# Kernel optimization log

Measured on AMD Instinct MI355X. Metric: run time of the kernel, lower is better.

## Reference

```python
import jax, jax.numpy as jnp
import numpy as np

N_NODES = 100000
N_EDGES = 1600000
DIM_IN, DIM_HID, DIM_OUT = 256, 128, 64


def _gcn_norm(edge_index, num_nodes):
    # PyG gcn_norm with add_self_loops=True, symmetric normalization.
    loop = jnp.arange(num_nodes, dtype=edge_index.dtype)
    row = jnp.concatenate([edge_index[0], loop])  # source
    col = jnp.concatenate([edge_index[1], loop])  # destination
    deg = jax.ops.segment_sum(jnp.ones_like(col, dtype=jnp.float32), col,
                              num_segments=num_nodes)
    dis = jnp.where(deg > 0, jax.lax.rsqrt(deg), 0.0)
    norm = dis[row] * dis[col]  # [E + N]
    return row, col, norm


def _gcn_conv(x, row, col, norm, W, b, num_nodes):
    h = x @ W                      # [N, d_out] linear first (d_out <= d_in typical)
    msg = h[row] * norm[:, None]   # gather + edge scaling, [E+N, d_out]
    out = jax.ops.segment_sum(msg, col, num_segments=num_nodes)  # scatter-add
    return out + b


def setup_inputs() -> dict:
    key = jax.random.key(0)
    k1, k2, k3, k4, k5 = jax.random.split(key, 5)
    x = jax.random.normal(k1, (N_NODES, DIM_IN), dtype=jnp.float32)
    edge_index = jax.random.randint(k2, (2, N_EDGES), 0, N_NODES, dtype=jnp.int32)
    s1 = 1.0 / np.sqrt(DIM_IN)
    s2 = 1.0 / np.sqrt(DIM_HID)
    W1 = jax.random.uniform(k3, (DIM_IN, DIM_HID), jnp.float32, -s1, s1)
    b1 = jnp.zeros((DIM_HID,), jnp.float32)
    W2 = jax.random.uniform(k4, (DIM_HID, DIM_OUT), jnp.float32, -s2, s2)
    b2 = jnp.zeros((DIM_OUT,), jnp.float32)
    return {"x": x, "edge_index": edge_index, "W1": W1, "b1": b1,
            "W2": W2, "b2": b2}


def reference(x, edge_index, W1, b1, W2, b2):
    n = x.shape[0]
    row, col, norm = _gcn_norm(edge_index, n)  # cached=True: shared by both layers
    h = _gcn_conv(x, row, col, norm, W1, b1, n)
    h = jax.nn.relu(h)
    h = _gcn_conv(h, row, col, norm, W2, b2, n)
    return jax.nn.log_softmax(h, axis=-1)
```

## Files before the change

### kernel.cpp

```cpp
#include <hip/hip_runtime.h>

#define N_NODES 100000
#define N_EDGES 1600000
#define DIN 256
#define DHID 128
#define DOUT 64

#define BSHIFT 8
#define NBUCKET ((N_NODES + 255) / 256)
#define CHUNK 4096
#define NCHUNK ((N_EDGES + CHUNK - 1) / CHUNK)

typedef __attribute__((ext_vector_type(8))) short bf16x8;
typedef __attribute__((ext_vector_type(4))) float f32x4;
typedef __attribute__((ext_vector_type(2))) float f32x2;

static __device__ __forceinline__ ushort f2bf(float f) {
  union { float f; uint u; } a; a.f = f;
  uint u = a.u;
  uint r = u + 0x7fffu + ((u >> 16) & 1u);
  return (ushort)(r >> 16);
}


#if __has_builtin(__builtin_amdgcn_cvt_pk_f32_fp8) && __has_builtin(__builtin_amdgcn_cvt_pk_fp8_f32) && __has_builtin(__builtin_amdgcn_cvt_f32_fp8)
#define FP8_HW 1
#else
#define FP8_HW 0
#endif

static __device__ __forceinline__ uint f2fp8(float f) {
#if FP8_HW
  return (uint)(__builtin_amdgcn_cvt_pk_fp8_f32(f, f, 0, false) & 0xFF);
#else
  uint u = __float_as_uint(f);
  uint s = (u >> 24) & 0x80u;
  u &= 0x7FFFFFFFu;
  u += 0x7FFFFu + ((u >> 20) & 1u);
  int e = (int)(u >> 23) - 120;
  uint m = (u >> 20) & 7u;
  uint v = (e <= 0) ? 0u : ((e >= 15) ? 0x7Eu : (((uint)e << 3) | m));
  return s | v;
#endif
}

static __device__ __forceinline__ f32x2 fp8x2f(uint v) {
#if FP8_HW
  return __builtin_amdgcn_cvt_pk_f32_fp8(v, false);
#else
  uint lo = v & 0xFFu, hi = (v >> 8) & 0xFFu;
  uint mlo = lo & 0x7Fu, mhi = hi & 0x7Fu;
  uint blo = (mlo ? ((mlo << 4) + 0x3C00u) : 0u) | ((lo & 0x80u) << 8);
  uint bhi = (mhi ? ((mhi << 4) + 0x3C00u) : 0u) | ((hi & 0x80u) << 8);
  f32x2 r;
  r.x = __uint_as_float(blo << 16);
  r.y = __uint_as_float(bhi << 16);
  return r;
#endif
}


__global__ __launch_bounds__(256) void k_hist(const int* __restrict__ colp,
                                              int* __restrict__ cntmat) {
  __shared__ int h[NBUCKET];
  int c = blockIdx.x;
  for (int i = threadIdx.x; i < NBUCKET; i += 256) h[i] = 0;
  __syncthreads();
  int e0 = c * CHUNK, e1 = min(e0 + CHUNK, N_EDGES);
  for (int e = e0 + threadIdx.x; e < e1; e += 256)
    atomicAdd(&h[colp[e] >> BSHIFT], 1);
  __syncthreads();
  for (int i = threadIdx.x; i < NBUCKET; i += 256)
    cntmat[c * NBUCKET + i] = h[i];
}


__global__ __launch_bounds__(256) void k_buckettot(const int* __restrict__ cntmat,
                                                   int* __restrict__ btot) {
  __shared__ int s[256];
  int b = blockIdx.x, t = threadIdx.x;
  int sum = 0;
  for (int c = t; c < NCHUNK; c += 256) sum += cntmat[c * NBUCKET + b];
  s[t] = sum;
  __syncthreads();
  for (int d = 128; d > 0; d >>= 1) {
    if (t < d) s[t] += s[t + d];
    __syncthreads();
  }
  if (t == 0) btot[b] = s[0];
}


__global__ void k_bucketscan(const int* __restrict__ btot, int* __restrict__ bbase) {
  __shared__ int s[256];
  int t = threadIdx.x;
  int b0 = 2 * t, b1 = 2 * t + 1;
  int v0 = (b0 < NBUCKET) ? btot[b0] : 0;
  int v1 = (b1 < NBUCKET) ? btot[b1] : 0;
  int ps = v0 + v1;
  s[t] = ps;
  __syncthreads();
  for (int d = 1; d < 256; d <<= 1) {
    int y = (t >= d) ? s[t - d] : 0;
    __syncthreads();
    s[t] += y;
    __syncthreads();
  }
  int ex = s[t] - ps;
  if (b0 < NBUCKET) bbase[b0] = ex;
  if (b1 < NBUCKET) bbase[b1] = ex + v0;
  if (t == 0) bbase[NBUCKET] = N_EDGES;
}


__global__ __launch_bounds__(256) void k_chunkpfx(const int* __restrict__ cntmat,
                                                  const int* __restrict__ bbase,
                                                  int* __restrict__ basemat) {
  int wid = blockIdx.x * 4 + (threadIdx.x >> 6);
  int lane = threadIdx.x & 63;
  if (wid >= NBUCKET) return;
  int carry = bbase[wid];
  const int NT = (NCHUNK + 63) / 64;
  for (int tt = 0; tt < NT; tt++) {
    int c = tt * 64 + lane;
    int v = (c < NCHUNK) ? cntmat[c * NBUCKET + wid] : 0;
    int incl = v;
#pragma unroll
    for (int d = 1; d < 64; d <<= 1) {
      int y = __shfl_up(incl, d, 64);
      if (lane >= d) incl += y;
    }
    if (c < NCHUNK) basemat[c * NBUCKET + wid] = carry + incl - v;
    carry += __shfl(incl, 63, 64);
  }
}


__global__ __launch_bounds__(256) void k_binscatter(const int* __restrict__ rowp,
                                                    const int* __restrict__ colp,
                                                    const int* __restrict__ basemat,
                                                    uint* __restrict__ packed) {
  __shared__ int lcur[NBUCKET];
  int c = blockIdx.x;
  for (int i = threadIdx.x; i < NBUCKET; i += 256)
    lcur[i] = basemat[c * NBUCKET + i];
  __syncthreads();
  int e0 = c * CHUNK, e1 = min(e0 + CHUNK, N_EDGES);
  for (int e = e0 + threadIdx.x; e < e1; e += 256) {
    int dst = colp[e], src = rowp[e];
    int pos = atomicAdd(&lcur[dst >> BSHIFT], 1);
    packed[pos] = (uint)src | ((uint)(dst & 255) << 17);
  }
}


__global__ __launch_bounds__(256) void k_count256(const uint* __restrict__ packed,
                                                  const int* __restrict__ bbase,
                                                  int* __restrict__ off,
                                                  float* __restrict__ dis) {
  __shared__ int cnt[256];
  __shared__ int s[256];
  int b = blockIdx.x, t = threadIdx.x;
  int node0 = b << BSHIFT;
  int nn = min(256, N_NODES - node0);
  cnt[t] = 0;
  __syncthreads();
  int r0 = bbase[b], r1 = bbase[b + 1];
  for (int r = r0 + t; r < r1; r += 256)
    atomicAdd(&cnt[packed[r] >> 17], 1);
  __syncthreads();
  int c = cnt[t];
  s[t] = c;
  __syncthreads();
  for (int d = 1; d < 256; d <<= 1) {
    int y = (t >= d) ? s[t - d] : 0;
    __syncthreads();
    s[t] += y;
    __syncthreads();
  }
  int ex = s[t] - c;
  if (t < nn) {
    off[node0 + t] = r0 + ex;
    dis[node0 + t] = rsqrtf((float)c + 1.0f);
  }
  if (b == NBUCKET - 1 && t == 0) off[N_NODES] = N_EDGES;
}


__global__ __launch_bounds__(256) void k_place(const uint* __restrict__ packed,
                                               const int* __restrict__ bbase,
                                               const int* __restrict__ off,
                                               const float* __restrict__ dis,
                                               uint* __restrict__ ep) {
  __shared__ int cur[256];
  __shared__ int offl[256];
  int b = blockIdx.x, t = threadIdx.x;
  int node0 = b << BSHIFT;
  int nn = min(256, N_NODES - node0);
  cur[t] = 0;
  if (t < nn) offl[t] = off[node0 + t];
  __syncthreads();
  int r0 = bbase[b], r1 = bbase[b + 1];
  for (int r = r0 + t; r < r1; r += 256) {
    uint sd = packed[r];
    int d0 = sd >> 17;
    uint src = sd & 0x1FFFFu;
    float w = dis[src];
    uint w15 = min((uint)(w * 32768.0f + 0.5f), 32767u);
    int pos = offl[d0] + atomicAdd(&cur[d0], 1);
    ep[pos] = src | (w15 << 17);
  }
}


__global__ void k_packW(const float* __restrict__ W1, ushort* __restrict__ Wp1,
                        const float* __restrict__ W2, ushort* __restrict__ Wp2) {
  int t = blockIdx.x * 256 + threadIdx.x;
  if (t < 8 * 8 * 64) {
    int l = t & 63, ks = (t >> 6) & 7, nt = t >> 9;
    int k0 = ks * 32 + (l >> 4) * 8;
    int n = nt * 16 + (l & 15);
    ushort* dst = Wp1 + (size_t)t * 8;
#pragma unroll
    for (int i = 0; i < 8; i++) dst[i] = f2bf(W1[(k0 + i) * DHID + n]);
  } else if (t < 8 * 8 * 64 + 4 * 4 * 64) {
    int t2 = t - 8 * 8 * 64;
    int l = t2 & 63, ks = (t2 >> 6) & 3, nt = t2 >> 8;
    int k0 = ks * 32 + (l >> 4) * 8;
    int n = nt * 16 + (l & 15);
    ushort* dst = Wp2 + (size_t)t2 * 8;
#pragma unroll
    for (int i = 0; i < 8; i++) dst[i] = f2bf(W2[(k0 + i) * DOUT + n]);
  }
}


__global__ __launch_bounds__(256) void k_gemm1(const float* __restrict__ x,
                                               const ushort* __restrict__ Wp,
                                               uchar* __restrict__ h1) {
  __shared__ uchar cs[4][16][144];
  int w = threadIdx.x >> 6, l = threadIdx.x & 63;
  int row0 = blockIdx.x * 64 + w * 16;
  bool valid = (row0 < N_NODES);
  if (valid) {
    f32x4 acc[8];
#pragma unroll
    for (int i = 0; i < 8; i++) acc[i] = (f32x4)(0.f);
    int arow = row0 + (l & 15);
    const float4* xg = (const float4*)(x + (size_t)arow * DIN) + (l >> 4) * 2;
    const bf16x8* wp = (const bf16x8*)Wp;
    float4 a[16];
#pragma unroll
    for (int ks = 0; ks < 8; ks++) {
      a[2 * ks]     = xg[ks * 8];
      a[2 * ks + 1] = xg[ks * 8 + 1];
    }
#pragma unroll
    for (int ks = 0; ks < 8; ks++) {
      float4 a0 = a[2 * ks];
      float4 a1 = a[2 * ks + 1];
      bf16x8 af;
      af[0] = (short)f2bf(a0.x); af[1] = (short)f2bf(a0.y);
      af[2] = (short)f2bf(a0.z); af[3] = (short)f2bf(a0.w);
      af[4] = (short)f2bf(a1.x); af[5] = (short)f2bf(a1.y);
      af[6] = (short)f2bf(a1.z); af[7] = (short)f2bf(a1.w);
#pragma unroll
      for (int nt = 0; nt < 8; nt++) {
        bf16x8 bf = wp[(nt * 8 + ks) * 64 + l];
        acc[nt] = __builtin_amdgcn_mfma_f32_16x16x32_bf16(af, bf, acc[nt], 0, 0, 0);
      }
    }
#pragma unroll
    for (int nt = 0; nt < 8; nt++)
#pragma unroll
      for (int r = 0; r < 4; r++)
        cs[w][(l >> 4) * 4 + r][nt * 16 + (l & 15)] = (uchar)f2fp8(acc[nt][r]);
  }
  __syncthreads();
  if (valid) {
    const uint4* s4 = (const uint4*)&cs[w][l >> 2][(l & 3) * 32];
    uint4* dst = (uint4*)(h1 + (size_t)(row0 + (l >> 2)) * DHID + (l & 3) * 32);
    dst[0] = s4[0]; dst[1] = s4[1];
  }
}


#define AGG1_BATCH4(eX, pfx)                                                    \
  {                                                                             \
    uint p0 = ep[eX], p1 = ep[eX + 1], p2 = ep[eX + 2], p3 = ep[eX + 3];        \
    ushort v0 = h1[(size_t)(p0 & 0x1FFFFu) * 64 + lane];                        \
    ushort v1 = h1[(size_t)(p1 & 0x1FFFFu) * 64 + lane];                        \
    ushort v2 = h1[(size_t)(p2 & 0x1FFFFu) * 64 + lane];                        \
    ushort v3 = h1[(size_t)(p3 & 0x1FFFFu) * 64 + lane];                        \
    f32x2 f0 = fp8x2f(v0), f1 = fp8x2f(v1), f2 = fp8x2f(v2), f3 = fp8x2f(v3);   \
    float w0 = (float)(p0 >> 17) * 0x1p-15f;                                    \
    float w1 = (float)(p1 >> 17) * 0x1p-15f;                                    \
    float w2 = (float)(p2 >> 17) * 0x1p-15f;                                    \
    float w3 = (float)(p3 >> 17) * 0x1p-15f;                                    \
    ax##pfx = fmaf(f0.x, w0, ax##pfx); ay##pfx = fmaf(f0.y, w0, ay##pfx);       \
    ax##pfx = fmaf(f1.x, w1, ax##pfx); ay##pfx = fmaf(f1.y, w1, ay##pfx);       \
    ax##pfx = fmaf(f2.x, w2, ax##pfx); ay##pfx = fmaf(f2.y, w2, ay##pfx);       \
    ax##pfx = fmaf(f3.x, w3, ax##pfx); ay##pfx = fmaf(f3.y, w3, ay##pfx);       \
  }

#define AGG1_TAIL(eX, eX1, pfx)                                                 \
  for (; eX < eX1; eX++) {                                                      \
    uint p = ep[eX];                                                            \
    f32x2 f0 = fp8x2f(h1[(size_t)(p & 0x1FFFFu) * 64 + lane]);                  \
    float w0 = (float)(p >> 17) * 0x1p-15f;                                     \
    ax##pfx = fmaf(f0.x, w0, ax##pfx); ay##pfx = fmaf(f0.y, w0, ay##pfx);       \
  }

__global__ __launch_bounds__(256) void k_agg1g2(const ushort* __restrict__ h1,
                                                const int* __restrict__ off,
                                                const uint* __restrict__ ep,
                                                const float* __restrict__ dis,
                                                const float* __restrict__ b1,
                                                const ushort* __restrict__ Wp2,
                                                uchar* __restrict__ h2) {
  __shared__ ushort as[16][136];
  int w = threadIdx.x >> 6, lane = threadIdx.x & 63;
  int nb0 = blockIdx.x * 16;
  float2 bb = ((const float2*)b1)[lane];
  int widA = nb0 + w * 4;
  float dA = dis[widA], dB = dis[widA + 1], dC = dis[widA + 2], dD = dis[widA + 3];
  f32x2 hvA = fp8x2f(h1[(size_t)widA * 64 + lane]);
  f32x2 hvB = fp8x2f(h1[(size_t)(widA + 1) * 64 + lane]);
  f32x2 hvC = fp8x2f(h1[(size_t)(widA + 2) * 64 + lane]);
  f32x2 hvD = fp8x2f(h1[(size_t)(widA + 3) * 64 + lane]);
  float axA = hvA.x * dA, ayA = hvA.y * dA;
  float axB = hvB.x * dB, ayB = hvB.y * dB;
  float axC = hvC.x * dC, ayC = hvC.y * dC;
  float axD = hvD.x * dD, ayD = hvD.y * dD;
  int eA  = __builtin_amdgcn_readfirstlane(off[widA]);
  int eA1 = __builtin_amdgcn_readfirstlane(off[widA + 1]);
  int eB  = eA1;
  int eB1 = __builtin_amdgcn_readfirstlane(off[widA + 2]);
  int eC  = eB1;
  int eC1 = __builtin_amdgcn_readfirstlane(off[widA + 3]);
  int eD  = eC1;
  int eD1 = __builtin_amdgcn_readfirstlane(off[widA + 4]);
  while (eA + 4 <= eA1 && eB + 4 <= eB1 && eC + 4 <= eC1 && eD + 4 <= eD1) {
    AGG1_BATCH4(eA, A)
    AGG1_BATCH4(eB, B)
    AGG1_BATCH4(eC, C)
    AGG1_BATCH4(eD, D)
    eA += 4; eB += 4; eC += 4; eD += 4;
  }
  while (eA + 4 <= eA1 && eB + 4 <= eB1) {
    AGG1_BATCH4(eA, A)
    AGG1_BATCH4(eB, B)
    eA += 4; eB += 4;
  }
  while (eC + 4 <= eC1 && eD + 4 <= eD1) {
    AGG1_BATCH4(eC, C)
    AGG1_BATCH4(eD, D)
    eC += 4; eD += 4;
  }
  for (; eA + 4 <= eA1; eA += 4) AGG1_BATCH4(eA, A)
  for (; eB + 4 <= eB1; eB += 4) AGG1_BATCH4(eB, B)
  for (; eC + 4 <= eC1; eC += 4) AGG1_BATCH4(eC, C)
  for (; eD + 4 <= eD1; eD += 4) AGG1_BATCH4(eD, D)
  AGG1_TAIL(eA, eA1, A)
  AGG1_TAIL(eB, eB1, B)
  AGG1_TAIL(eC, eC1, C)
  AGG1_TAIL(eD, eD1, D)
  {
    float rx, ry;
    rx = fmaxf(fmaf(dA, axA, bb.x), 0.f); ry = fmaxf(fmaf(dA, ayA, bb.y), 0.f);
    ((uint*)&as[w * 4 + 0][0])[lane] = (uint)f2bf(rx) | ((uint)f2bf(ry) << 16);
    rx = fmaxf(fmaf(dB, axB, bb.x), 0.f); ry = fmaxf(fmaf(dB, ayB, bb.y), 0.f);
    ((uint*)&as[w * 4 + 1][0])[lane] = (uint)f2bf(rx) | ((uint)f2bf(ry) << 16);
    rx = fmaxf(fmaf(dC, axC, bb.x), 0.f); ry = fmaxf(fmaf(dC, ayC, bb.y), 0.f);
    ((uint*)&as[w * 4 + 2][0])[lane] = (uint)f2bf(rx) | ((uint)f2bf(ry) << 16);
    rx = fmaxf(fmaf(dD, axD, bb.x), 0.f); ry = fmaxf(fmaf(dD, ayD, bb.y), 0.f);
    ((uint*)&as[w * 4 + 3][0])[lane] = (uint)f2bf(rx) | ((uint)f2bf(ry) << 16);
  }
  __syncthreads();
  f32x4 acc = (f32x4)(0.f);
  const bf16x8* wp = (const bf16x8*)Wp2;
#pragma unroll
  for (int ks = 0; ks < 4; ks++) {
    bf16x8 af = *(const bf16x8*)&as[lane & 15][ks * 32 + (lane >> 4) * 8];
    bf16x8 bf = wp[(w * 4 + ks) * 64 + lane];
    acc = __builtin_amdgcn_mfma_f32_16x16x32_bf16(af, bf, acc, 0, 0, 0);
  }
#pragma unroll
  for (int r = 0; r < 4; r++) {
    int row = (lane >> 4) * 4 + r;
    h2[(size_t)(nb0 + row) * DOUT + w * 16 + (lane & 15)] = (uchar)f2fp8(acc[r]);
  }
}


#define AGG2_BATCH4(eX)                                                         \
  {                                                                             \
    uint p0 = ep[eX], p1 = ep[eX + 1], p2 = ep[eX + 2], p3 = ep[eX + 3];        \
    uint v0 = h2u[(size_t)(p0 & 0x1FFFFu) * 16 + q];                            \
    uint v1 = h2u[(size_t)(p1 & 0x1FFFFu) * 16 + q];                            \
    uint v2 = h2u[(size_t)(p2 & 0x1FFFFu) * 16 + q];                            \
    uint v3 = h2u[(size_t)(p3 & 0x1FFFFu) * 16 + q];                            \
    float w0 = (float)(p0 >> 17) * 0x1p-15f;                                    \
    float w1 = (float)(p1 >> 17) * 0x1p-15f;                                    \
    float w2 = (float)(p2 >> 17) * 0x1p-15f;                                    \
    float w3 = (float)(p3 >> 17) * 0x1p-15f;                                    \
    f32x2 l0 = fp8x2f(v0), h0 = fp8x2f(v0 >> 16);                               \
    f32x2 l1 = fp8x2f(v1), h1_ = fp8x2f(v1 >> 16);                              \
    f32x2 l2 = fp8x2f(v2), h2_ = fp8x2f(v2 >> 16);                              \
    f32x2 l3 = fp8x2f(v3), h3_ = fp8x2f(v3 >> 16);                              \
    a0 = fmaf(l0.x, w0, a0); a1 = fmaf(l0.y, w0, a1);                           \
    a2 = fmaf(h0.x, w0, a2); a3 = fmaf(h0.y, w0, a3);                           \
    a0 = fmaf(l1.x, w1, a0); a1 = fmaf(l1.y, w1, a1);                           \
    a2 = fmaf(h1_.x, w1, a2); a3 = fmaf(h1_.y, w1, a3);                         \
    a0 = fmaf(l2.x, w2, a0); a1 = fmaf(l2.y, w2, a1);                           \
    a2 = fmaf(h2_.x, w2, a2); a3 = fmaf(h2_.y, w2, a3);                         \
    a0 = fmaf(l3.x, w3, a0); a1 = fmaf(l3.y, w3, a1);                           \
    a2 = fmaf(h3_.x, w3, a2); a3 = fmaf(h3_.y, w3, a3);                         \
  }

__global__ __launch_bounds__(256) void k_agg2(const uint* __restrict__ h2u,
                                              const int* __restrict__ off,
                                              const uint* __restrict__ ep,
                                              const float* __restrict__ dis,
                                              const float* __restrict__ b2,
                                              float* __restrict__ out) {
  int gw   = (blockIdx.x * 256 + threadIdx.x) >> 6;
  int lane = threadIdx.x & 63;
  int g = lane >> 4;
  int q = lane & 15;
  int wid = gw * 4 + g;
  if (wid >= N_NODES) return;
  float d = dis[wid];
  uint sv = h2u[(size_t)wid * 16 + q];
  f32x2 slo = fp8x2f(sv), shi = fp8x2f(sv >> 16);
  float a0 = slo.x * d, a1 = slo.y * d, a2 = shi.x * d, a3 = shi.y * d;
  int o0 = off[wid], o1 = off[wid + 1];
  int e = o0;
  for (; e + 4 <= o1; e += 4) AGG2_BATCH4(e)
  for (; e < o1; e++) {
    uint p = ep[e];
    uint v = h2u[(size_t)(p & 0x1FFFFu) * 16 + q];
    float w = (float)(p >> 17) * 0x1p-15f;
    f32x2 lo = fp8x2f(v), hi = fp8x2f(v >> 16);
    a0 = fmaf(lo.x, w, a0); a1 = fmaf(lo.y, w, a1);
    a2 = fmaf(hi.x, w, a2); a3 = fmaf(hi.y, w, a3);
  }
  float4 bbv = ((const float4*)b2)[q];
  float v0 = fmaf(d, a0, bbv.x);
  float v1 = fmaf(d, a1, bbv.y);
  float v2 = fmaf(d, a2, bbv.z);
  float v3 = fmaf(d, a3, bbv.w);
  float m = fmaxf(fmaxf(v0, v1), fmaxf(v2, v3));
#pragma unroll
  for (int sft = 8; sft >= 1; sft >>= 1) m = fmaxf(m, __shfl_xor(m, sft, 64));
  float sum = expf(v0 - m) + expf(v1 - m) + expf(v2 - m) + expf(v3 - m);
#pragma unroll
  for (int sft = 8; sft >= 1; sft >>= 1) sum += __shfl_xor(sum, sft, 64);
  float ls = m + logf(sum);
  float4 o;
  o.x = v0 - ls; o.y = v1 - ls; o.z = v2 - ls; o.w = v3 - ls;
  ((float4*)out)[(size_t)wid * 16 + q] = o;
}


extern "C" void kernel_launch(void* const* d_in, const int* in_sizes, int n_in,
                              void* d_out, int out_size, void* d_ws, size_t ws_size,
                              hipStream_t stream) {
  const float* x  = (const float*)d_in[0];
  const int*   ei = (const int*)d_in[1];
  const float* W1 = (const float*)d_in[2];
  const float* b1 = (const float*)d_in[3];
  const float* W2 = (const float*)d_in[4];
  const float* b2 = (const float*)d_in[5];
  float* out = (float*)d_out;
  const int* rowp = ei;
  const int* colp = ei + N_EDGES;

  char* p = (char*)d_ws;
  size_t o = 0;
  auto alloc = [&](size_t bytes) -> void* {
    void* r = p + o;
    o = (o + bytes + 255) & ~(size_t)255;
    return r;
  };
  int*    off    = (int*)alloc((size_t)(N_NODES + 1) * 4);
  float*  dis    = (float*)alloc((size_t)N_NODES * 4);
  int*    cntmat = (int*)alloc((size_t)NCHUNK * NBUCKET * 4);
  int*    basemat= (int*)alloc((size_t)NCHUNK * NBUCKET * 4);
  int*    btot   = (int*)alloc((size_t)NBUCKET * 4);
  int*    bbase  = (int*)alloc((size_t)(NBUCKET + 1) * 4);
  uint*   packed = (uint*)alloc((size_t)N_EDGES * 4);
  uint*   ep     = (uint*)alloc((size_t)N_EDGES * 4);
  ushort* Wp1    = (ushort*)alloc((size_t)8 * 8 * 64 * 8 * 2);
  ushort* Wp2    = (ushort*)alloc((size_t)4 * 4 * 64 * 8 * 2);
  uchar*  h1     = (uchar*)alloc((size_t)N_NODES * DHID);
  uchar*  h2     = (uchar*)alloc((size_t)N_NODES * DOUT);

  k_hist<<<NCHUNK, 256, 0, stream>>>(colp, cntmat);
  k_buckettot<<<NBUCKET, 256, 0, stream>>>(cntmat, btot);
  k_bucketscan<<<1, 256, 0, stream>>>(btot, bbase);
  k_chunkpfx<<<(NBUCKET + 3) / 4, 256, 0, stream>>>(cntmat, bbase, basemat);
  k_binscatter<<<NCHUNK, 256, 0, stream>>>(rowp, colp, basemat, packed);
  k_count256<<<NBUCKET, 256, 0, stream>>>(packed, bbase, off, dis);
  k_place<<<NBUCKET, 256, 0, stream>>>(packed, bbase, off, dis, ep);
  k_packW<<<20, 256, 0, stream>>>(W1, Wp1, W2, Wp2);
  k_gemm1<<<(N_NODES + 63) / 64, 256, 0, stream>>>(x, Wp1, h1);
  k_agg1g2<<<N_NODES / 16, 256, 0, stream>>>((const ushort*)h1, off, ep, dis, b1, Wp2, h2);
  k_agg2<<<N_NODES / 16, 256, 0, stream>>>((const uint*)h2, off, ep, dis, b2, out);
}
```

Baseline: 159.7 us.

## Fuse bucket scan into chunk prefix, halve chunk size, fold weight scale

Merges the single-block bucket scan into the chunk-prefix kernel: every block redundantly recomputes the bucket scan in shared memory, and block 0 writes bbase out. This removes one launch and one dependent step. The edge chunk size is halved, which doubles the number of histogram and binscatter blocks and the size of the count matrix. The per-edge 2^-15 weight scaling is moved out of the inner aggregation loops into the self-loop initialisation and the final output scaling, saving one multiply per edge.

```diff
diff --git a/kernel.cpp b/kernel.cpp
--- a/kernel.cpp
+++ b/kernel.cpp
@@ -8,7 +8,7 @@
 
 #define BSHIFT 8
 #define NBUCKET ((N_NODES + 255) / 256)
-#define CHUNK 4096
+#define CHUNK 2048
 #define NCHUNK ((N_EDGES + CHUNK - 1) / CHUNK)
 
 typedef __attribute__((ext_vector_type(8))) short bf16x8;
@@ -91,8 +91,12 @@
 }
 
 
-__global__ void k_bucketscan(const int* __restrict__ btot, int* __restrict__ bbase) {
+__global__ __launch_bounds__(256) void k_chunkpfx(const int* __restrict__ cntmat,
+                                                  const int* __restrict__ btot,
+                                                  int* __restrict__ bbase,
+                                                  int* __restrict__ basemat) {
   __shared__ int s[256];
+  __shared__ int bb[NBUCKET + 1];
   int t = threadIdx.x;
   int b0 = 2 * t, b1 = 2 * t + 1;
   int v0 = (b0 < NBUCKET) ? btot[b0] : 0;
@@ -107,19 +111,17 @@
     __syncthreads();
   }
   int ex = s[t] - ps;
-  if (b0 < NBUCKET) bbase[b0] = ex;
-  if (b1 < NBUCKET) bbase[b1] = ex + v0;
-  if (t == 0) bbase[NBUCKET] = N_EDGES;
-}
-
-
-__global__ __launch_bounds__(256) void k_chunkpfx(const int* __restrict__ cntmat,
-                                                  const int* __restrict__ bbase,
-                                                  int* __restrict__ basemat) {
-  int wid = blockIdx.x * 4 + (threadIdx.x >> 6);
-  int lane = threadIdx.x & 63;
+  if (b0 < NBUCKET) bb[b0] = ex;
+  if (b1 < NBUCKET) bb[b1] = ex + v0;
+  if (t == 0) bb[NBUCKET] = N_EDGES;
+  __syncthreads();
+  if (blockIdx.x == 0) {
+    for (int i = t; i <= NBUCKET; i += 256) bbase[i] = bb[i];
+  }
+  int wid = blockIdx.x * 4 + (t >> 6);
+  int lane = t & 63;
   if (wid >= NBUCKET) return;
-  int carry = bbase[wid];
+  int carry = bb[wid];
   const int NT = (NCHUNK + 63) / 64;
   for (int tt = 0; tt < NT; tt++) {
     int c = tt * 64 + lane;
@@ -293,10 +295,10 @@
     ushort v2 = h1[(size_t)(p2 & 0x1FFFFu) * 64 + lane];                        \
     ushort v3 = h1[(size_t)(p3 & 0x1FFFFu) * 64 + lane];                        \
     f32x2 f0 = fp8x2f(v0), f1 = fp8x2f(v1), f2 = fp8x2f(v2), f3 = fp8x2f(v3);   \
-    float w0 = (float)(p0 >> 17) * 0x1p-15f;                                    \
-    float w1 = (float)(p1 >> 17) * 0x1p-15f;                                    \
-    float w2 = (float)(p2 >> 17) * 0x1p-15f;                                    \
-    float w3 = (float)(p3 >> 17) * 0x1p-15f;                                    \
+    float w0 = (float)(p0 >> 17);                                               \
+    float w1 = (float)(p1 >> 17);                                               \
+    float w2 = (float)(p2 >> 17);                                               \
+    float w3 = (float)(p3 >> 17);                                               \
     ax##pfx = fmaf(f0.x, w0, ax##pfx); ay##pfx = fmaf(f0.y, w0, ay##pfx);       \
     ax##pfx = fmaf(f1.x, w1, ax##pfx); ay##pfx = fmaf(f1.y, w1, ay##pfx);       \
     ax##pfx = fmaf(f2.x, w2, ax##pfx); ay##pfx = fmaf(f2.y, w2, ay##pfx);       \
@@ -307,7 +309,7 @@
   for (; eX < eX1; eX++) {                                                      \
     uint p = ep[eX];                                                            \
     f32x2 f0 = fp8x2f(h1[(size_t)(p & 0x1FFFFu) * 64 + lane]);                  \
-    float w0 = (float)(p >> 17) * 0x1p-15f;                                     \
+    float w0 = (float)(p >> 17);                                                \
     ax##pfx = fmaf(f0.x, w0, ax##pfx); ay##pfx = fmaf(f0.y, w0, ay##pfx);       \
   }
 
@@ -328,10 +330,11 @@
   f32x2 hvB = fp8x2f(h1[(size_t)(widA + 1) * 64 + lane]);
   f32x2 hvC = fp8x2f(h1[(size_t)(widA + 2) * 64 + lane]);
   f32x2 hvD = fp8x2f(h1[(size_t)(widA + 3) * 64 + lane]);
-  float axA = hvA.x * dA, ayA = hvA.y * dA;
-  float axB = hvB.x * dB, ayB = hvB.y * dB;
-  float axC = hvC.x * dC, ayC = hvC.y * dC;
-  float axD = hvD.x * dD, ayD = hvD.y * dD;
+  float sA = dA * 32768.0f, sB = dB * 32768.0f, sC = dC * 32768.0f, sD = dD * 32768.0f;
+  float axA = hvA.x * sA, ayA = hvA.y * sA;
+  float axB = hvB.x * sB, ayB = hvB.y * sB;
+  float axC = hvC.x * sC, ayC = hvC.y * sC;
+  float axD = hvD.x * sD, ayD = hvD.y * sD;
   int eA  = __builtin_amdgcn_readfirstlane(off[widA]);
   int eA1 = __builtin_amdgcn_readfirstlane(off[widA + 1]);
   int eB  = eA1;
@@ -367,13 +370,14 @@
   AGG1_TAIL(eD, eD1, D)
   {
     float rx, ry;
-    rx = fmaxf(fmaf(dA, axA, bb.x), 0.f); ry = fmaxf(fmaf(dA, ayA, bb.y), 0.f);
+    float fA = dA * 0x1p-15f, fB = dB * 0x1p-15f, fC = dC * 0x1p-15f, fD = dD * 0x1p-15f;
+    rx = fmaxf(fmaf(fA, axA, bb.x), 0.f); ry = fmaxf(fmaf(fA, ayA, bb.y), 0.f);
     ((uint*)&as[w * 4 + 0][0])[lane] = (uint)f2bf(rx) | ((uint)f2bf(ry) << 16);
-    rx = fmaxf(fmaf(dB, axB, bb.x), 0.f); ry = fmaxf(fmaf(dB, ayB, bb.y), 0.f);
+    rx = fmaxf(fmaf(fB, axB, bb.x), 0.f); ry = fmaxf(fmaf(fB, ayB, bb.y), 0.f);
     ((uint*)&as[w * 4 + 1][0])[lane] = (uint)f2bf(rx) | ((uint)f2bf(ry) << 16);
-    rx = fmaxf(fmaf(dC, axC, bb.x), 0.f); ry = fmaxf(fmaf(dC, ayC, bb.y), 0.f);
+    rx = fmaxf(fmaf(fC, axC, bb.x), 0.f); ry = fmaxf(fmaf(fC, ayC, bb.y), 0.f);
     ((uint*)&as[w * 4 + 2][0])[lane] = (uint)f2bf(rx) | ((uint)f2bf(ry) << 16);
-    rx = fmaxf(fmaf(dD, axD, bb.x), 0.f); ry = fmaxf(fmaf(dD, ayD, bb.y), 0.f);
+    rx = fmaxf(fmaf(fD, axD, bb.x), 0.f); ry = fmaxf(fmaf(fD, ayD, bb.y), 0.f);
     ((uint*)&as[w * 4 + 3][0])[lane] = (uint)f2bf(rx) | ((uint)f2bf(ry) << 16);
   }
   __syncthreads();
@@ -400,10 +404,10 @@
     uint v1 = h2u[(size_t)(p1 & 0x1FFFFu) * 16 + q];                            \
     uint v2 = h2u[(size_t)(p2 & 0x1FFFFu) * 16 + q];                            \
     uint v3 = h2u[(size_t)(p3 & 0x1FFFFu) * 16 + q];                            \
-    float w0 = (float)(p0 >> 17) * 0x1p-15f;                                    \
-    float w1 = (float)(p1 >> 17) * 0x1p-15f;                                    \
-    float w2 = (float)(p2 >> 17) * 0x1p-15f;                                    \
-    float w3 = (float)(p3 >> 17) * 0x1p-15f;                                    \
+    float w0 = (float)(p0 >> 17);                                               \
+    float w1 = (float)(p1 >> 17);                                               \
+    float w2 = (float)(p2 >> 17);                                               \
+    float w3 = (float)(p3 >> 17);                                               \
     f32x2 l0 = fp8x2f(v0), h0 = fp8x2f(v0 >> 16);                               \
     f32x2 l1 = fp8x2f(v1), h1_ = fp8x2f(v1 >> 16);                              \
     f32x2 l2 = fp8x2f(v2), h2_ = fp8x2f(v2 >> 16);                              \
@@ -433,23 +437,25 @@
   float d = dis[wid];
   uint sv = h2u[(size_t)wid * 16 + q];
   f32x2 slo = fp8x2f(sv), shi = fp8x2f(sv >> 16);
-  float a0 = slo.x * d, a1 = slo.y * d, a2 = shi.x * d, a3 = shi.y * d;
+  float dS = d * 32768.0f;
+  float a0 = slo.x * dS, a1 = slo.y * dS, a2 = shi.x * dS, a3 = shi.y * dS;
   int o0 = off[wid], o1 = off[wid + 1];
   int e = o0;
   for (; e + 4 <= o1; e += 4) AGG2_BATCH4(e)
   for (; e < o1; e++) {
     uint p = ep[e];
     uint v = h2u[(size_t)(p & 0x1FFFFu) * 16 + q];
-    float w = (float)(p >> 17) * 0x1p-15f;
+    float w = (float)(p >> 17);
     f32x2 lo = fp8x2f(v), hi = fp8x2f(v >> 16);
     a0 = fmaf(lo.x, w, a0); a1 = fmaf(lo.y, w, a1);
     a2 = fmaf(hi.x, w, a2); a3 = fmaf(hi.y, w, a3);
   }
   float4 bbv = ((const float4*)b2)[q];
-  float v0 = fmaf(d, a0, bbv.x);
-  float v1 = fmaf(d, a1, bbv.y);
-  float v2 = fmaf(d, a2, bbv.z);
-  float v3 = fmaf(d, a3, bbv.w);
+  float ds = d * 0x1p-15f;
+  float v0 = fmaf(ds, a0, bbv.x);
+  float v1 = fmaf(ds, a1, bbv.y);
+  float v2 = fmaf(ds, a2, bbv.z);
+  float v3 = fmaf(ds, a3, bbv.w);
   float m = fmaxf(fmaxf(v0, v1), fmaxf(v2, v3));
 #pragma unroll
   for (int sft = 8; sft >= 1; sft >>= 1) m = fmaxf(m, __shfl_xor(m, sft, 64));
@@ -498,8 +504,7 @@
 
   k_hist<<<NCHUNK, 256, 0, stream>>>(colp, cntmat);
   k_buckettot<<<NBUCKET, 256, 0, stream>>>(cntmat, btot);
-  k_bucketscan<<<1, 256, 0, stream>>>(btot, bbase);
-  k_chunkpfx<<<(NBUCKET + 3) / 4, 256, 0, stream>>>(cntmat, bbase, basemat);
+  k_chunkpfx<<<(NBUCKET + 3) / 4, 256, 0, stream>>>(cntmat, btot, bbase, basemat);
   k_binscatter<<<NCHUNK, 256, 0, stream>>>(rowp, colp, basemat, packed);
   k_count256<<<NBUCKET, 256, 0, stream>>>(packed, bbase, off, dis);
   k_place<<<NBUCKET, 256, 0, stream>>>(packed, bbase, off, dis, ep);
```

Result: slower. 163.9 us (+2.6%).
